# Optimization experiments

Hardware: AMD Instinct MI355X
Metric: run time of the kernel (lower is better)

The kernel has to match this reference:

```python
import jax, jax.numpy as jnp
import numpy as np

B, H, S, DK = 4, 16, 2048, 64


def setup_inputs() -> dict:
    key = jax.random.key(0)
    kq, kk, kv, km = jax.random.split(key, 4)
    Q = jax.random.normal(kq, (B, H, S, DK), dtype=jnp.float32)
    K = jax.random.normal(kk, (B, H, S, DK), dtype=jnp.float32)
    V = jax.random.normal(kv, (B, H, S, DK), dtype=jnp.float32)
    mask = (jax.random.uniform(km, (B, 1, S, S)) > 0.1).astype(jnp.float32)
    return {"Q": Q, "K": K, "V": V, "mask": mask}


def reference(Q, K, V, mask):
    d_k = Q.shape[-1]
    # unnormalized exp scores (no max subtraction), multiplicative mask
    scores = jnp.exp(jnp.einsum("bhqd,bhkd->bhqk", Q, K) / jnp.sqrt(jnp.float32(d_k)))
    scores = scores * mask
    attn = scores / (jnp.sum(scores, axis=-1, keepdims=True) + 1e-8)
    return jnp.einsum("bhqk,bhkd->bhqd", attn, V)
```

## Files before the change

### kernel.cpp

```cpp
#include <hip/hip_runtime.h>

namespace {
constexpr int S  = 2048;
constexpr int D  = 64;
constexpr int BQ = 256;
constexpr int BK = 64;
constexpr int NT = 512;
constexpr int NKT = S / BK;

typedef short bf16x8 __attribute__((ext_vector_type(8)));
typedef float f32x4  __attribute__((ext_vector_type(4)));

__device__ inline unsigned short bf16c(float x) {
  __bf16 h = (__bf16)x;
  return __builtin_bit_cast(unsigned short, h);
}
__device__ inline unsigned pk2(float a, float b) {
  return (unsigned)bf16c(a) | ((unsigned)bf16c(b) << 16);
}
__device__ inline void gld_lds16(const void* g, void* l) {
  __builtin_amdgcn_global_load_lds(
      (const __attribute__((address_space(1))) unsigned int*)g,
      (__attribute__((address_space(3))) unsigned int*)l, 16, 0, 0);
}
#if __has_builtin(__builtin_amdgcn_exp2f)
__device__ inline float exp2v(float x) { return __builtin_amdgcn_exp2f(x); }
#else
__device__ inline float exp2v(float x) { return __expf(x * 0.6931471805599453f); }
#endif

__device__ inline int kswz_of_row(int row) {
  return (row & 3) | (((row >> 3) & 1) << 2);
}

__device__ inline bf16x8 mk_pa(f32x4 s0, f32x4 s1, unsigned mw0, unsigned mw1) {
  float p0 = exp2v(s0[0]) * (float)(mw0 & 0xffu);
  float p1 = exp2v(s0[1]) * (float)((mw0 >> 8) & 0xffu);
  float p2 = exp2v(s0[2]) * (float)((mw0 >> 16) & 0xffu);
  float p3 = exp2v(s0[3]) * (float)(mw0 >> 24);
  float p4 = exp2v(s1[0]) * (float)(mw1 & 0xffu);
  float p5 = exp2v(s1[1]) * (float)((mw1 >> 8) & 0xffu);
  float p6 = exp2v(s1[2]) * (float)((mw1 >> 16) & 0xffu);
  float p7 = exp2v(s1[3]) * (float)(mw1 >> 24);
  uint4 u = make_uint4(pk2(p0, p1), pk2(p2, p3), pk2(p4, p5), pk2(p6, p7));
  return __builtin_bit_cast(bf16x8, u);
}

__global__ __launch_bounds__(512) void prep_all(
    const float* __restrict__ K, const float* __restrict__ V,
    const float* __restrict__ M, unsigned short* __restrict__ Kws,
    unsigned short* __restrict__ Vws, unsigned char* __restrict__ M2) {
  __shared__ __align__(16) unsigned char smem[51200];
  const int blk = blockIdx.x;
  const int t   = threadIdx.x;

  if (blk < 2048) {
    int gid = blk * 512 + t;
    int row = gid >> 3;
    int g   = gid & 7;
    const float* src = K + (size_t)row * 64 + g * 8;
    float4 a = *(const float4*)src;
    float4 b = *(const float4*)(src + 4);
    uint4 w;
    w.x = pk2(a.x, a.y); w.y = pk2(a.z, a.w);
    w.z = pk2(b.x, b.y); w.w = pk2(b.z, b.w);
    *(uint4*)(Kws + (size_t)row * 64 + ((g ^ kswz_of_row(row)) * 8)) = w;
  } else if (blk < 3072) {
    const int half = t >> 8;
    const int tsub = t & 255;
    const size_t tile = (size_t)(blk - 2048) * 2 + half;
    float* tl = (float*)smem + half * (64 * 68);
    unsigned short* so = (unsigned short*)(smem + 34816) + half * 4096;
    const float* src = V + tile * (64 * 64);
#pragma unroll
    for (int rep = 0; rep < 4; ++rep) {
      int idx = tsub + rep * 256;
      int row = idx >> 4, d4 = idx & 15;
      float4 v = *(const float4*)(src + row * 64 + d4 * 4);
      *(float4*)(tl + row * 68 + d4 * 4) = v;
    }
    __syncthreads();
#pragma unroll
    for (int rep = 0; rep < 2; ++rep) {
      int d  = (tsub & 31) + rep * 32;
      int kg = tsub >> 5;
      float x[8];
#pragma unroll
      for (int j = 0; j < 8; ++j) x[j] = tl[(kg * 8 + j) * 68 + d];
      uint4 w;
      w.x = pk2(x[0], x[1]); w.y = pk2(x[2], x[3]);
      w.z = pk2(x[4], x[5]); w.w = pk2(x[6], x[7]);
      *(uint4*)(so + d * 64 + ((kg ^ (d & 7)) * 8)) = w;
    }
    __syncthreads();
    unsigned short* dstT = Vws + tile * (64 * 64);
#pragma unroll
    for (int rep = 0; rep < 2; ++rep) {
      int i = tsub + rep * 256;
      *(uint4*)(dstT + i * 8) = *(const uint4*)(so + i * 8);
    }
  } else {
    unsigned (*nibs)[129] = (unsigned (*)[129])smem;
    const int bqg = blk - 3072;
    const int b  = bqg >> 6;
    const int qg = bqg & 63;
    const float* src = M + ((size_t)b * S + (size_t)qg * 32) * S;
#pragma unroll
    for (int pass = 0; pass < 8; ++pass) {
      int idx = pass * 512 + t;
      int q  = idx >> 7;
      int kc = idx & 127;
      const float* p = src + (size_t)q * S + kc * 16;
      unsigned w = 0;
#pragma unroll
      for (int j = 0; j < 4; ++j) {
        float4 v = *(const float4*)(p + j * 4);
        unsigned nib = (v.x != 0.f ? 1u : 0u) | (v.y != 0.f ? 2u : 0u) |
                       (v.z != 0.f ? 4u : 0u) | (v.w != 0.f ? 8u : 0u);
        w |= nib << (8 * j);
      }
      nibs[q][kc] = w;
    }
    __syncthreads();
    const int e    = t & 127;
    const int lane = e >> 1, g = e & 1;
    const int n16  = lane & 15, quad = lane >> 4;
    const int qq   = g * 16 + n16;
    const int c    = quad >> 1;
    const int sh0  = 8 * ((2 * quad) & 3);
    unsigned char* dstb = M2 + ((size_t)b * NKT * 64 + qg) * 2048 + (size_t)e * 16;
#pragma unroll
    for (int i = 0; i < 8; ++i) {
      int kt = (t >> 7) + i * 4;
      unsigned d0 = nibs[qq][kt * 4 + c];
      unsigned d1 = nibs[qq][kt * 4 + 2 + c];
      unsigned n00 = (d0 >> sh0) & 0xFu;
      unsigned n01 = (d0 >> (sh0 + 8)) & 0xFu;
      unsigned n10 = (d1 >> sh0) & 0xFu;
      unsigned n11 = (d1 >> (sh0 + 8)) & 0xFu;
      uint4 out;
      out.x = (n00 * 0x00204081u) & 0x01010101u;
      out.y = (n01 * 0x00204081u) & 0x01010101u;
      out.z = (n10 * 0x00204081u) & 0x01010101u;
      out.w = (n11 * 0x00204081u) & 0x01010101u;
      *(uint4*)(dstb + (size_t)kt * (64 * 64 * 32)) = out;
    }
  }
}

__global__ __launch_bounds__(NT, 4)
void attn3(const float* __restrict__ Qg, const unsigned char* __restrict__ M2,
           const unsigned short* __restrict__ Kws,
           const unsigned short* __restrict__ Vws,
           float* __restrict__ Og) {
  __shared__ __align__(16) unsigned short sK[2][BK * D];
  __shared__ __align__(16) unsigned short sV[2][BK * D];

  const int t    = threadIdx.x;
  const int wave = t >> 6;
  const int lane = t & 63;
  const int quad = lane >> 4;
  const int n16  = lane & 15;

  const int bh = blockIdx.y;
  const int b  = bh >> 4;
  const int q0 = blockIdx.x * BQ;
  const int qg = blockIdx.x * 8 + wave;

  const unsigned short* Kb = Kws + (size_t)bh * S * D;
  const unsigned short* Vb = Vws + (size_t)bh * S * D;
  const unsigned char* Mp = M2 + (((size_t)b * NKT * 64 + qg) * 64 + lane) * 32;
  constexpr size_t MKT = (size_t)64 * 64 * 32;

  const int h2 = n16 >> 2, rr = n16 & 3;
  const int krow0 = (8 * h2 + rr) * 64;

  const int sw = n16 & 7;
  const int ga = (quad ^ sw) * 8;
  const int gb = ((quad + 4) ^ sw) * 8;

  constexpr float QS = 0.18033688011112042f;
  const float* QbA = Qg + ((size_t)bh * S + q0 + wave * 32 + n16) * D;
  bf16x8 aqA[2], aqB[2];
#pragma unroll
  for (int ks = 0; ks < 2; ++ks) {
    const float* qp = QbA + ks * 32 + quad * 8;
    float4 x = *(const float4*)qp;
    float4 y = *(const float4*)(qp + 4);
    bf16x8 a;
    a[0] = (short)bf16c(x.x * QS); a[1] = (short)bf16c(x.y * QS);
    a[2] = (short)bf16c(x.z * QS); a[3] = (short)bf16c(x.w * QS);
    a[4] = (short)bf16c(y.x * QS); a[5] = (short)bf16c(y.y * QS);
    a[6] = (short)bf16c(y.z * QS); a[7] = (short)bf16c(y.w * QS);
    aqA[ks] = a;
    const float* qp2 = qp + 16 * D;
    float4 x2 = *(const float4*)qp2;
    float4 y2 = *(const float4*)(qp2 + 4);
    bf16x8 a2;
    a2[0] = (short)bf16c(x2.x * QS); a2[1] = (short)bf16c(x2.y * QS);
    a2[2] = (short)bf16c(x2.z * QS); a2[3] = (short)bf16c(x2.w * QS);
    a2[4] = (short)bf16c(y2.x * QS); a2[5] = (short)bf16c(y2.y * QS);
    a2[6] = (short)bf16c(y2.z * QS); a2[7] = (short)bf16c(y2.w * QS);
    aqB[ks] = a2;
  }

  bf16x8 ones;
#pragma unroll
  for (int i = 0; i < 8; ++i) ones[i] = (short)0x3F80;

  f32x4 oA[4], oB[4];
#pragma unroll
  for (int nt = 0; nt < 4; ++nt) {
    oA[nt] = (f32x4){0.f, 0.f, 0.f, 0.f};
    oB[nt] = (f32x4){0.f, 0.f, 0.f, 0.f};
  }
  f32x4 rsA = (f32x4){0.f, 0.f, 0.f, 0.f};
  f32x4 rsB = (f32x4){0.f, 0.f, 0.f, 0.f};

  gld_lds16(Kb + wave * 512 + lane * 8, &sK[0][wave * 512]);
  gld_lds16(Vb + wave * 512 + lane * 8, &sV[0][wave * 512]);
  uint4 mkA[2], mkB[2];
  mkA[0] = *(const uint4*)Mp;
  mkB[0] = *(const uint4*)(Mp + 16);

#pragma unroll 2
  for (int kt = 0; kt < NKT; ++kt) {
    const int cur = kt & 1, nxt = cur ^ 1;
    __syncthreads();

    if (kt + 1 < NKT) {
      gld_lds16(Kb + (size_t)(kt + 1) * (BK * D) + wave * 512 + lane * 8,
                &sK[nxt][wave * 512]);
      gld_lds16(Vb + (size_t)(kt + 1) * (BK * D) + wave * 512 + lane * 8,
                &sV[nxt][wave * 512]);
      mkA[nxt] = *(const uint4*)(Mp + (size_t)(kt + 1) * MKT);
      mkB[nxt] = *(const uint4*)(Mp + (size_t)(kt + 1) * MKT + 16);
    }

    bf16x8 paA[2], paB[2];
#pragma unroll
    for (int ks = 0; ks < 2; ++ks) {
      const unsigned short* base = &sK[cur][krow0 + ks * 2048];
      bf16x8 k0a = *(const bf16x8*)(base + ga);
      bf16x8 k0b = *(const bf16x8*)(base + gb);
      bf16x8 k1a = *(const bf16x8*)(base + 256 + ga);
      bf16x8 k1b = *(const bf16x8*)(base + 256 + gb);
      const f32x4 z = (f32x4){0.f, 0.f, 0.f, 0.f};

      f32x4 sA0 = __builtin_amdgcn_mfma_f32_16x16x32_bf16(k0a, aqA[0], z, 0, 0, 0);
      sA0 = __builtin_amdgcn_mfma_f32_16x16x32_bf16(k0b, aqA[1], sA0, 0, 0, 0);
      f32x4 sA1 = __builtin_amdgcn_mfma_f32_16x16x32_bf16(k1a, aqA[0], z, 0, 0, 0);
      sA1 = __builtin_amdgcn_mfma_f32_16x16x32_bf16(k1b, aqA[1], sA1, 0, 0, 0);
      paA[ks] = mk_pa(sA0, sA1, ks ? mkA[cur].z : mkA[cur].x,
                                ks ? mkA[cur].w : mkA[cur].y);

      f32x4 sB0 = __builtin_amdgcn_mfma_f32_16x16x32_bf16(k0a, aqB[0], z, 0, 0, 0);
      sB0 = __builtin_amdgcn_mfma_f32_16x16x32_bf16(k0b, aqB[1], sB0, 0, 0, 0);
      f32x4 sB1 = __builtin_amdgcn_mfma_f32_16x16x32_bf16(k1a, aqB[0], z, 0, 0, 0);
      sB1 = __builtin_amdgcn_mfma_f32_16x16x32_bf16(k1b, aqB[1], sB1, 0, 0, 0);
      paB[ks] = mk_pa(sB0, sB1, ks ? mkB[cur].z : mkB[cur].x,
                                ks ? mkB[cur].w : mkB[cur].y);
    }

    __builtin_amdgcn_s_setprio(1);
    rsA = __builtin_amdgcn_mfma_f32_16x16x32_bf16(ones, paA[0], rsA, 0, 0, 0);
    rsA = __builtin_amdgcn_mfma_f32_16x16x32_bf16(ones, paA[1], rsA, 0, 0, 0);
    rsB = __builtin_amdgcn_mfma_f32_16x16x32_bf16(ones, paB[0], rsB, 0, 0, 0);
    rsB = __builtin_amdgcn_mfma_f32_16x16x32_bf16(ones, paB[1], rsB, 0, 0, 0);

#pragma unroll
    for (int nt = 0; nt < 4; ++nt) {
      const int row = nt * 16 + n16;
      bf16x8 v0 = *(const bf16x8*)(sV[cur] + row * 64 + ga);
      bf16x8 v1 = *(const bf16x8*)(sV[cur] + row * 64 + gb);
      oA[nt] = __builtin_amdgcn_mfma_f32_16x16x32_bf16(v0, paA[0], oA[nt], 0, 0, 0);
      oA[nt] = __builtin_amdgcn_mfma_f32_16x16x32_bf16(v1, paA[1], oA[nt], 0, 0, 0);
      oB[nt] = __builtin_amdgcn_mfma_f32_16x16x32_bf16(v0, paB[0], oB[nt], 0, 0, 0);
      oB[nt] = __builtin_amdgcn_mfma_f32_16x16x32_bf16(v1, paB[1], oB[nt], 0, 0, 0);
    }
    __builtin_amdgcn_s_setprio(0);
  }

  const float invA = 1.0f / (rsA[0] + 1e-8f);
  const float invB = 1.0f / (rsB[0] + 1e-8f);
  float* OA = Og + ((size_t)bh * S + q0 + wave * 32 + n16) * D;
#pragma unroll
  for (int nt = 0; nt < 4; ++nt) {
    float4 wa = make_float4(oA[nt][0] * invA, oA[nt][1] * invA,
                            oA[nt][2] * invA, oA[nt][3] * invA);
    *(float4*)(OA + nt * 16 + quad * 4) = wa;
    float4 wb = make_float4(oB[nt][0] * invB, oB[nt][1] * invB,
                            oB[nt][2] * invB, oB[nt][3] * invB);
    *(float4*)(OA + 16 * D + nt * 16 + quad * 4) = wb;
  }
}
}

extern "C" void kernel_launch(void* const* d_in, const int* in_sizes, int n_in,
                              void* d_out, int out_size, void* d_ws, size_t ws_size,
                              hipStream_t stream) {
  const float* Q = (const float*)d_in[0];
  const float* K = (const float*)d_in[1];
  const float* V = (const float*)d_in[2];
  const float* M = (const float*)d_in[3];
  float* O = (float*)d_out;

  unsigned short* Kws = (unsigned short*)d_ws;
  unsigned short* Vws = Kws + (size_t)64 * S * D;
  unsigned char*  M2  = (unsigned char*)(Vws + (size_t)64 * S * D);

  prep_all<<<dim3(3328), 512, 0, stream>>>(K, V, M, Kws, Vws, M2);
  attn3<<<dim3(S / BQ, 64), NT, 0, stream>>>(Q, M2, Kws, Vws, O);
}
```

Before: 276.2 us.

## Fuse prep and attention into one persistent kernel with grid barrier

Merges the K/V/mask preprocessing kernel into the attention kernel. The 512 attention blocks first share out the prep work (mask packing on 256 blocks, K/V conversion on the rest), then synchronize through a global atomic counter before running attention. This removes a kernel launch and its boundary, at the cost of a memset, a spin barrier that deadlocks unless all 512 blocks are co-resident, and less balanced prep work. It also drops the s_setprio hints around the MFMA block.

```diff
diff --git a/kernel.cpp b/kernel.cpp
--- a/kernel.cpp
+++ b/kernel.cpp
@@ -7,6 +7,7 @@
 constexpr int BK = 64;
 constexpr int NT = 512;
 constexpr int NKT = S / BK;
+constexpr int NBLK = 512;
 
 typedef short bf16x8 __attribute__((ext_vector_type(8)));
 typedef float f32x4  __attribute__((ext_vector_type(4)));
@@ -46,64 +47,20 @@
   return __builtin_bit_cast(bf16x8, u);
 }
 
-__global__ __launch_bounds__(512) void prep_all(
-    const float* __restrict__ K, const float* __restrict__ V,
-    const float* __restrict__ M, unsigned short* __restrict__ Kws,
-    unsigned short* __restrict__ Vws, unsigned char* __restrict__ M2) {
+__global__ __launch_bounds__(NT, 4)
+void fused(const float* __restrict__ Qg, const float* __restrict__ K,
+           const float* __restrict__ V, const float* __restrict__ M,
+           unsigned short* __restrict__ Kws, unsigned short* __restrict__ Vws,
+           unsigned char* __restrict__ M2, unsigned* __restrict__ cnt,
+           float* __restrict__ Og) {
   __shared__ __align__(16) unsigned char smem[51200];
-  const int blk = blockIdx.x;
   const int t   = threadIdx.x;
-
-  if (blk < 2048) {
-    int gid = blk * 512 + t;
-    int row = gid >> 3;
-    int g   = gid & 7;
-    const float* src = K + (size_t)row * 64 + g * 8;
-    float4 a = *(const float4*)src;
-    float4 b = *(const float4*)(src + 4);
-    uint4 w;
-    w.x = pk2(a.x, a.y); w.y = pk2(a.z, a.w);
-    w.z = pk2(b.x, b.y); w.w = pk2(b.z, b.w);
-    *(uint4*)(Kws + (size_t)row * 64 + ((g ^ kswz_of_row(row)) * 8)) = w;
-  } else if (blk < 3072) {
-    const int half = t >> 8;
-    const int tsub = t & 255;
-    const size_t tile = (size_t)(blk - 2048) * 2 + half;
-    float* tl = (float*)smem + half * (64 * 68);
-    unsigned short* so = (unsigned short*)(smem + 34816) + half * 4096;
-    const float* src = V + tile * (64 * 64);
-#pragma unroll
-    for (int rep = 0; rep < 4; ++rep) {
-      int idx = tsub + rep * 256;
-      int row = idx >> 4, d4 = idx & 15;
-      float4 v = *(const float4*)(src + row * 64 + d4 * 4);
-      *(float4*)(tl + row * 68 + d4 * 4) = v;
-    }
-    __syncthreads();
-#pragma unroll
-    for (int rep = 0; rep < 2; ++rep) {
-      int d  = (tsub & 31) + rep * 32;
-      int kg = tsub >> 5;
-      float x[8];
-#pragma unroll
-      for (int j = 0; j < 8; ++j) x[j] = tl[(kg * 8 + j) * 68 + d];
-      uint4 w;
-      w.x = pk2(x[0], x[1]); w.y = pk2(x[2], x[3]);
-      w.z = pk2(x[4], x[5]); w.w = pk2(x[6], x[7]);
-      *(uint4*)(so + d * 64 + ((kg ^ (d & 7)) * 8)) = w;
-    }
-    __syncthreads();
-    unsigned short* dstT = Vws + tile * (64 * 64);
-#pragma unroll
-    for (int rep = 0; rep < 2; ++rep) {
-      int i = tsub + rep * 256;
-      *(uint4*)(dstT + i * 8) = *(const uint4*)(so + i * 8);
-    }
-  } else {
+  const int blk = blockIdx.y * 8 + blockIdx.x;
+
+  if (blk < 256) {
     unsigned (*nibs)[129] = (unsigned (*)[129])smem;
-    const int bqg = blk - 3072;
-    const int b  = bqg >> 6;
-    const int qg = bqg & 63;
+    const int b  = blk >> 6;
+    const int qg = blk & 63;
     const float* src = M + ((size_t)b * S + (size_t)qg * 32) * S;
 #pragma unroll
     for (int pass = 0; pass < 8; ++pass) {
@@ -145,18 +102,74 @@
       out.w = (n11 * 0x00204081u) & 0x01010101u;
       *(uint4*)(dstb + (size_t)kt * (64 * 64 * 32)) = out;
     }
-  }
-}
-
-__global__ __launch_bounds__(NT, 4)
-void attn3(const float* __restrict__ Qg, const unsigned char* __restrict__ M2,
-           const unsigned short* __restrict__ Kws,
-           const unsigned short* __restrict__ Vws,
-           float* __restrict__ Og) {
-  __shared__ __align__(16) unsigned short sK[2][BK * D];
-  __shared__ __align__(16) unsigned short sV[2][BK * D];
-
-  const int t    = threadIdx.x;
+  } else {
+    const int bb = blk - 256;
+#pragma unroll
+    for (int r = 0; r < 8; ++r) {
+      int gid = (bb * 8 + r) * 512 + t;
+      int row = gid >> 3;
+      int g   = gid & 7;
+      const float* src = K + (size_t)row * 64 + g * 8;
+      float4 a = *(const float4*)src;
+      float4 b4 = *(const float4*)(src + 4);
+      uint4 w;
+      w.x = pk2(a.x, a.y);  w.y = pk2(a.z, a.w);
+      w.z = pk2(b4.x, b4.y); w.w = pk2(b4.z, b4.w);
+      *(uint4*)(Kws + (size_t)row * 64 + ((g ^ kswz_of_row(row)) * 8)) = w;
+    }
+    const int half = t >> 8;
+    const int tsub = t & 255;
+    float* tl = (float*)smem + half * (64 * 68);
+    unsigned short* so = (unsigned short*)(smem + 34816) + half * 4096;
+    for (int r = 0; r < 4; ++r) {
+      const size_t tile = (size_t)(bb * 4 + r) * 2 + half;
+      const float* src = V + tile * (64 * 64);
+      __syncthreads();
+#pragma unroll
+      for (int rep = 0; rep < 4; ++rep) {
+        int idx = tsub + rep * 256;
+        int row = idx >> 4, d4 = idx & 15;
+        float4 v = *(const float4*)(src + row * 64 + d4 * 4);
+        *(float4*)(tl + row * 68 + d4 * 4) = v;
+      }
+      __syncthreads();
+#pragma unroll
+      for (int rep = 0; rep < 2; ++rep) {
+        int d  = (tsub & 31) + rep * 32;
+        int kg = tsub >> 5;
+        float x[8];
+#pragma unroll
+        for (int j = 0; j < 8; ++j) x[j] = tl[(kg * 8 + j) * 68 + d];
+        uint4 w;
+        w.x = pk2(x[0], x[1]); w.y = pk2(x[2], x[3]);
+        w.z = pk2(x[4], x[5]); w.w = pk2(x[6], x[7]);
+        *(uint4*)(so + d * 64 + ((kg ^ (d & 7)) * 8)) = w;
+      }
+      __syncthreads();
+      unsigned short* dstT = Vws + tile * (64 * 64);
+#pragma unroll
+      for (int rep = 0; rep < 2; ++rep) {
+        int i = tsub + rep * 256;
+        *(uint4*)(dstT + i * 8) = *(const uint4*)(so + i * 8);
+      }
+    }
+  }
+
+  __syncthreads();
+  __threadfence();
+  if (t == 0) {
+    __hip_atomic_fetch_add(cnt, 1u, __ATOMIC_ACQ_REL, __HIP_MEMORY_SCOPE_AGENT);
+    while (__hip_atomic_load(cnt, __ATOMIC_ACQUIRE, __HIP_MEMORY_SCOPE_AGENT)
+           < (unsigned)NBLK) {
+      __builtin_amdgcn_s_sleep(2);
+    }
+  }
+  __syncthreads();
+  __threadfence();
+
+  unsigned short (*sK)[BK * D] = (unsigned short (*)[BK * D])smem;
+  unsigned short (*sV)[BK * D] = (unsigned short (*)[BK * D])(smem + 16384);
+
   const int wave = t >> 6;
   const int lane = t & 63;
   const int quad = lane >> 4;
@@ -262,7 +275,6 @@
                                 ks ? mkB[cur].w : mkB[cur].y);
     }
 
-    __builtin_amdgcn_s_setprio(1);
     rsA = __builtin_amdgcn_mfma_f32_16x16x32_bf16(ones, paA[0], rsA, 0, 0, 0);
     rsA = __builtin_amdgcn_mfma_f32_16x16x32_bf16(ones, paA[1], rsA, 0, 0, 0);
     rsB = __builtin_amdgcn_mfma_f32_16x16x32_bf16(ones, paB[0], rsB, 0, 0, 0);
@@ -278,7 +290,6 @@
       oB[nt] = __builtin_amdgcn_mfma_f32_16x16x32_bf16(v0, paB[0], oB[nt], 0, 0, 0);
       oB[nt] = __builtin_amdgcn_mfma_f32_16x16x32_bf16(v1, paB[1], oB[nt], 0, 0, 0);
     }
-    __builtin_amdgcn_s_setprio(0);
   }
 
   const float invA = 1.0f / (rsA[0] + 1e-8f);
@@ -308,7 +319,8 @@
   unsigned short* Kws = (unsigned short*)d_ws;
   unsigned short* Vws = Kws + (size_t)64 * S * D;
   unsigned char*  M2  = (unsigned char*)(Vws + (size_t)64 * S * D);
-
-  prep_all<<<dim3(3328), 512, 0, stream>>>(K, V, M, Kws, Vws, M2);
-  attn3<<<dim3(S / BQ, 64), NT, 0, stream>>>(Q, M2, Kws, Vws, O);
-}
+  unsigned* cnt = (unsigned*)(M2 + (size_t)4 * NKT * 64 * 2048);
+
+  hipMemsetAsync(cnt, 0, sizeof(unsigned), stream);
+  fused<<<dim3(S / BQ, 64), NT, 0, stream>>>(Q, K, V, M, Kws, Vws, M2, cnt, O);
+}
```

New measurement: 599.5 us. 117% more time.

## Split prep kernel by operand and apply mask as bitwise AND on bf16

Applied to the files above, without the earlier changes.

The fused prep kernel is split into three kernels for K, V and the mask. This lets the K kernel run at 256 threads without the large shared-memory allocation that limited its occupancy. The mask is now stored as 0xFF bytes, so in the attention loop the probabilities are masked by ANDing the packed bf16 pairs with byte-permuted mask words instead of doing float multiplies per element. The s_setprio hints around the MFMA section are also removed. In exchange the change adds two extra kernel launches.

```diff
diff --git a/kernel.cpp b/kernel.cpp
--- a/kernel.cpp
+++ b/kernel.cpp
@@ -34,117 +34,113 @@
 }
 
 __device__ inline bf16x8 mk_pa(f32x4 s0, f32x4 s1, unsigned mw0, unsigned mw1) {
-  float p0 = exp2v(s0[0]) * (float)(mw0 & 0xffu);
-  float p1 = exp2v(s0[1]) * (float)((mw0 >> 8) & 0xffu);
-  float p2 = exp2v(s0[2]) * (float)((mw0 >> 16) & 0xffu);
-  float p3 = exp2v(s0[3]) * (float)(mw0 >> 24);
-  float p4 = exp2v(s1[0]) * (float)(mw1 & 0xffu);
-  float p5 = exp2v(s1[1]) * (float)((mw1 >> 8) & 0xffu);
-  float p6 = exp2v(s1[2]) * (float)((mw1 >> 16) & 0xffu);
-  float p7 = exp2v(s1[3]) * (float)(mw1 >> 24);
-  uint4 u = make_uint4(pk2(p0, p1), pk2(p2, p3), pk2(p4, p5), pk2(p6, p7));
+  uint4 u;
+  u.x = pk2(exp2v(s0[0]), exp2v(s0[1])) & __builtin_amdgcn_perm(0u, mw0, 0x01010000u);
+  u.y = pk2(exp2v(s0[2]), exp2v(s0[3])) & __builtin_amdgcn_perm(0u, mw0, 0x03030202u);
+  u.z = pk2(exp2v(s1[0]), exp2v(s1[1])) & __builtin_amdgcn_perm(0u, mw1, 0x01010000u);
+  u.w = pk2(exp2v(s1[2]), exp2v(s1[3])) & __builtin_amdgcn_perm(0u, mw1, 0x03030202u);
   return __builtin_bit_cast(bf16x8, u);
 }
 
-__global__ __launch_bounds__(512) void prep_all(
-    const float* __restrict__ K, const float* __restrict__ V,
-    const float* __restrict__ M, unsigned short* __restrict__ Kws,
-    unsigned short* __restrict__ Vws, unsigned char* __restrict__ M2) {
+__global__ __launch_bounds__(256) void prep_k(const float* __restrict__ K,
+                                              unsigned short* __restrict__ Kws) {
+  int gid = blockIdx.x * 256 + threadIdx.x;
+  int row = gid >> 3;
+  int g   = gid & 7;
+  const float* src = K + (size_t)row * 64 + g * 8;
+  float4 a = *(const float4*)src;
+  float4 b = *(const float4*)(src + 4);
+  uint4 w;
+  w.x = pk2(a.x, a.y); w.y = pk2(a.z, a.w);
+  w.z = pk2(b.x, b.y); w.w = pk2(b.z, b.w);
+  *(uint4*)(Kws + (size_t)row * 64 + ((g ^ kswz_of_row(row)) * 8)) = w;
+}
+
+__global__ __launch_bounds__(512) void prep_v(const float* __restrict__ V,
+                                              unsigned short* __restrict__ Vws) {
   __shared__ __align__(16) unsigned char smem[51200];
-  const int blk = blockIdx.x;
-  const int t   = threadIdx.x;
-
-  if (blk < 2048) {
-    int gid = blk * 512 + t;
-    int row = gid >> 3;
-    int g   = gid & 7;
-    const float* src = K + (size_t)row * 64 + g * 8;
-    float4 a = *(const float4*)src;
-    float4 b = *(const float4*)(src + 4);
+  const int t    = threadIdx.x;
+  const int half = t >> 8;
+  const int tsub = t & 255;
+  const size_t tile = (size_t)blockIdx.x * 2 + half;
+  float* tl = (float*)smem + half * (64 * 68);
+  unsigned short* so = (unsigned short*)(smem + 34816) + half * 4096;
+  const float* src = V + tile * (64 * 64);
+#pragma unroll
+  for (int rep = 0; rep < 4; ++rep) {
+    int idx = tsub + rep * 256;
+    int row = idx >> 4, d4 = idx & 15;
+    float4 v = *(const float4*)(src + row * 64 + d4 * 4);
+    *(float4*)(tl + row * 68 + d4 * 4) = v;
+  }
+  __syncthreads();
+#pragma unroll
+  for (int rep = 0; rep < 2; ++rep) {
+    int d  = (tsub & 31) + rep * 32;
+    int kg = tsub >> 5;
+    float x[8];
+#pragma unroll
+    for (int j = 0; j < 8; ++j) x[j] = tl[(kg * 8 + j) * 68 + d];
     uint4 w;
-    w.x = pk2(a.x, a.y); w.y = pk2(a.z, a.w);
-    w.z = pk2(b.x, b.y); w.w = pk2(b.z, b.w);
-    *(uint4*)(Kws + (size_t)row * 64 + ((g ^ kswz_of_row(row)) * 8)) = w;
-  } else if (blk < 3072) {
-    const int half = t >> 8;
-    const int tsub = t & 255;
-    const size_t tile = (size_t)(blk - 2048) * 2 + half;
-    float* tl = (float*)smem + half * (64 * 68);
-    unsigned short* so = (unsigned short*)(smem + 34816) + half * 4096;
-    const float* src = V + tile * (64 * 64);
-#pragma unroll
-    for (int rep = 0; rep < 4; ++rep) {
-      int idx = tsub + rep * 256;
-      int row = idx >> 4, d4 = idx & 15;
-      float4 v = *(const float4*)(src + row * 64 + d4 * 4);
-      *(float4*)(tl + row * 68 + d4 * 4) = v;
+    w.x = pk2(x[0], x[1]); w.y = pk2(x[2], x[3]);
+    w.z = pk2(x[4], x[5]); w.w = pk2(x[6], x[7]);
+    *(uint4*)(so + d * 64 + ((kg ^ (d & 7)) * 8)) = w;
+  }
+  __syncthreads();
+  unsigned short* dstT = Vws + tile * (64 * 64);
+#pragma unroll
+  for (int rep = 0; rep < 2; ++rep) {
+    int i = tsub + rep * 256;
+    *(uint4*)(dstT + i * 8) = *(const uint4*)(so + i * 8);
+  }
+}
+
+__global__ __launch_bounds__(512) void prep_m(const float* __restrict__ M,
+                                              unsigned char* __restrict__ M2) {
+  __shared__ unsigned nibs[32][129];
+  const int t  = threadIdx.x;
+  const int b  = blockIdx.x >> 6;
+  const int qg = blockIdx.x & 63;
+  const float* src = M + ((size_t)b * S + (size_t)qg * 32) * S;
+#pragma unroll
+  for (int pass = 0; pass < 8; ++pass) {
+    int idx = pass * 512 + t;
+    int q  = idx >> 7;
+    int kc = idx & 127;
+    const float* p = src + (size_t)q * S + kc * 16;
+    unsigned w = 0;
+#pragma unroll
+    for (int j = 0; j < 4; ++j) {
+      float4 v = *(const float4*)(p + j * 4);
+      unsigned nib = (v.x != 0.f ? 1u : 0u) | (v.y != 0.f ? 2u : 0u) |
+                     (v.z != 0.f ? 4u : 0u) | (v.w != 0.f ? 8u : 0u);
+      w |= nib << (8 * j);
     }
-    __syncthreads();
-#pragma unroll
-    for (int rep = 0; rep < 2; ++rep) {
-      int d  = (tsub & 31) + rep * 32;
-      int kg = tsub >> 5;
-      float x[8];
-#pragma unroll
-      for (int j = 0; j < 8; ++j) x[j] = tl[(kg * 8 + j) * 68 + d];
-      uint4 w;
-      w.x = pk2(x[0], x[1]); w.y = pk2(x[2], x[3]);
-      w.z = pk2(x[4], x[5]); w.w = pk2(x[6], x[7]);
-      *(uint4*)(so + d * 64 + ((kg ^ (d & 7)) * 8)) = w;
-    }
-    __syncthreads();
-    unsigned short* dstT = Vws + tile * (64 * 64);
-#pragma unroll
-    for (int rep = 0; rep < 2; ++rep) {
-      int i = tsub + rep * 256;
-      *(uint4*)(dstT + i * 8) = *(const uint4*)(so + i * 8);
-    }
-  } else {
-    unsigned (*nibs)[129] = (unsigned (*)[129])smem;
-    const int bqg = blk - 3072;
-    const int b  = bqg >> 6;
-    const int qg = bqg & 63;
-    const float* src = M + ((size_t)b * S + (size_t)qg * 32) * S;
-#pragma unroll
-    for (int pass = 0; pass < 8; ++pass) {
-      int idx = pass * 512 + t;
-      int q  = idx >> 7;
-      int kc = idx & 127;
-      const float* p = src + (size_t)q * S + kc * 16;
-      unsigned w = 0;
-#pragma unroll
-      for (int j = 0; j < 4; ++j) {
-        float4 v = *(const float4*)(p + j * 4);
-        unsigned nib = (v.x != 0.f ? 1u : 0u) | (v.y != 0.f ? 2u : 0u) |
-                       (v.z != 0.f ? 4u : 0u) | (v.w != 0.f ? 8u : 0u);
-        w |= nib << (8 * j);
-      }
-      nibs[q][kc] = w;
-    }
-    __syncthreads();
-    const int e    = t & 127;
-    const int lane = e >> 1, g = e & 1;
-    const int n16  = lane & 15, quad = lane >> 4;
-    const int qq   = g * 16 + n16;
-    const int c    = quad >> 1;
-    const int sh0  = 8 * ((2 * quad) & 3);
-    unsigned char* dstb = M2 + ((size_t)b * NKT * 64 + qg) * 2048 + (size_t)e * 16;
-#pragma unroll
-    for (int i = 0; i < 8; ++i) {
-      int kt = (t >> 7) + i * 4;
-      unsigned d0 = nibs[qq][kt * 4 + c];
-      unsigned d1 = nibs[qq][kt * 4 + 2 + c];
-      unsigned n00 = (d0 >> sh0) & 0xFu;
-      unsigned n01 = (d0 >> (sh0 + 8)) & 0xFu;
-      unsigned n10 = (d1 >> sh0) & 0xFu;
-      unsigned n11 = (d1 >> (sh0 + 8)) & 0xFu;
-      uint4 out;
-      out.x = (n00 * 0x00204081u) & 0x01010101u;
-      out.y = (n01 * 0x00204081u) & 0x01010101u;
-      out.z = (n10 * 0x00204081u) & 0x01010101u;
-      out.w = (n11 * 0x00204081u) & 0x01010101u;
-      *(uint4*)(dstb + (size_t)kt * (64 * 64 * 32)) = out;
-    }
+    nibs[q][kc] = w;
+  }
+  __syncthreads();
+  const int e    = t & 127;
+  const int lane = e >> 1, g = e & 1;
+  const int n16  = lane & 15, quad = lane >> 4;
+  const int qq   = g * 16 + n16;
+  const int c    = quad >> 1;
+  const int sh0  = 8 * ((2 * quad) & 3);
+  unsigned char* dstb = M2 + ((size_t)b * NKT * 64 + qg) * 2048 + (size_t)e * 16;
+#pragma unroll
+  for (int i = 0; i < 8; ++i) {
+    int kt = (t >> 7) + i * 4;
+    unsigned d0 = nibs[qq][kt * 4 + c];
+    unsigned d1 = nibs[qq][kt * 4 + 2 + c];
+    unsigned n00 = (d0 >> sh0) & 0xFu;
+    unsigned n01 = (d0 >> (sh0 + 8)) & 0xFu;
+    unsigned n10 = (d1 >> sh0) & 0xFu;
+    unsigned n11 = (d1 >> (sh0 + 8)) & 0xFu;
+    uint4 out;
+    out.x = ((n00 * 0x00204081u) & 0x01010101u) * 255u;
+    out.y = ((n01 * 0x00204081u) & 0x01010101u) * 255u;
+    out.z = ((n10 * 0x00204081u) & 0x01010101u) * 255u;
+    out.w = ((n11 * 0x00204081u) & 0x01010101u) * 255u;
+    *(uint4*)(dstb + (size_t)kt * (64 * 64 * 32)) = out;
   }
 }
 
@@ -262,7 +258,6 @@
                                 ks ? mkB[cur].w : mkB[cur].y);
     }
 
-    __builtin_amdgcn_s_setprio(1);
     rsA = __builtin_amdgcn_mfma_f32_16x16x32_bf16(ones, paA[0], rsA, 0, 0, 0);
     rsA = __builtin_amdgcn_mfma_f32_16x16x32_bf16(ones, paA[1], rsA, 0, 0, 0);
     rsB = __builtin_amdgcn_mfma_f32_16x16x32_bf16(ones, paB[0], rsB, 0, 0, 0);
@@ -278,7 +273,6 @@
       oB[nt] = __builtin_amdgcn_mfma_f32_16x16x32_bf16(v0, paB[0], oB[nt], 0, 0, 0);
       oB[nt] = __builtin_amdgcn_mfma_f32_16x16x32_bf16(v1, paB[1], oB[nt], 0, 0, 0);
     }
-    __builtin_amdgcn_s_setprio(0);
   }
 
   const float invA = 1.0f / (rsA[0] + 1e-8f);
@@ -309,6 +303,8 @@
   unsigned short* Vws = Kws + (size_t)64 * S * D;
   unsigned char*  M2  = (unsigned char*)(Vws + (size_t)64 * S * D);
 
-  prep_all<<<dim3(3328), 512, 0, stream>>>(K, V, M, Kws, Vws, M2);
+  prep_k<<<dim3(64 * S * D / 8 / 256), 256, 0, stream>>>(K, Kws);
+  prep_v<<<dim3(64 * NKT / 2), 512, 0, stream>>>(V, Vws);
+  prep_m<<<dim3(4 * 64), 512, 0, stream>>>(M, M2);
   attn3<<<dim3(S / BQ, 64), NT, 0, stream>>>(Q, M2, Kws, Vws, O);
 }
```

New measurement: 268.6 us. 1.03x faster.
